# Kernel optimization log

Measured on AMD Instinct MI355X. Metric: run time of the kernel, lower is better.

## Reference

```python
import jax, jax.numpy as jnp
import numpy as np

KH = KW = 3
STRIDE = 1
PAD = 1
DIL = 1


def _conv2d(x, w, b):
    out = jax.lax.conv_general_dilated(
        x, w, (STRIDE, STRIDE), [(PAD, PAD), (PAD, PAD)],
        rhs_dilation=(DIL, DIL), dimension_numbers=('NCHW', 'OIHW', 'NCHW'))
    return out + b[None, :, None, None]


def _bilinear_sample(x, ys, xs):
    # x: [B,C,H,W]; ys, xs: [B,K,Ho,Wo] float sampling coords (zero padding outside)
    B, C, H, W = x.shape
    y0 = jnp.floor(ys)
    x0 = jnp.floor(xs)
    wy1 = ys - y0
    wx1 = xs - x0
    wy0 = 1.0 - wy1
    wx0 = 1.0 - wx1
    x_flat = x.reshape(B, C, H * W)

    def gather(yc, xc):
        valid = (yc >= 0) & (yc <= H - 1) & (xc >= 0) & (xc <= W - 1)
        yi = jnp.clip(yc, 0, H - 1).astype(jnp.int32)
        xi = jnp.clip(xc, 0, W - 1).astype(jnp.int32)
        idx = yi * W + xi  # [B,K,Ho,Wo]
        g = jax.vmap(lambda xb, ib: xb[:, ib.reshape(-1)])(x_flat, idx)
        g = g.reshape(B, C, *idx.shape[1:])  # [B,C,K,Ho,Wo]
        return g * valid[:, None].astype(x.dtype)

    return (gather(y0, x0) * (wy0 * wx0)[:, None]
            + gather(y0, x0 + 1) * (wy0 * wx1)[:, None]
            + gather(y0 + 1, x0) * (wy1 * wx0)[:, None]
            + gather(y0 + 1, x0 + 1) * (wy1 * wx1)[:, None])


def setup_inputs() -> dict:
    key = jax.random.key(0)
    ks = jax.random.split(key, 6)
    B, C, H, W = 8, 256, 64, 64
    Cout = 256
    K = KH * KW
    x = jax.random.normal(ks[0], (B, C, H, W), jnp.float32)
    # small random offset/mask heads (module inits them to zero; random keeps the
    # irregular-gather path exercised with modest, realistic offsets)
    w_offset = jax.random.normal(ks[1], (2 * K, C, KH, KW), jnp.float32) * 0.01
    b_offset = jax.random.normal(ks[2], (2 * K,), jnp.float32) * 0.1
    w_mask = jax.random.normal(ks[3], (K, C, KH, KW), jnp.float32) * 0.01
    b_mask = jnp.zeros((K,), jnp.float32)
    stdv = 1.0 / np.sqrt(C * KH * KW)
    weight = jax.random.uniform(ks[4], (Cout, C, KH, KW), jnp.float32, -stdv, stdv)
    bias = jnp.zeros((Cout,), jnp.float32)
    return {"x": x, "w_offset": w_offset, "b_offset": b_offset,
            "w_mask": w_mask, "b_mask": b_mask, "weight": weight, "bias": bias}


def reference(x, w_offset, b_offset, w_mask, b_mask, weight, bias):
    B, C, H, W = x.shape
    K = KH * KW
    offset = _conv2d(x, w_offset, b_offset)          # [B, 2K, Ho, Wo]
    mask = jax.nn.sigmoid(_conv2d(x, w_mask, b_mask))  # [B, K, Ho, Wo]
    Ho, Wo = offset.shape[2], offset.shape[3]
    off = offset.reshape(B, K, 2, Ho, Wo)
    dy, dx = off[:, :, 0], off[:, :, 1]              # (dy, dx) pairs per kernel tap
    ky = jnp.arange(KH, dtype=x.dtype) * DIL - PAD
    kx = jnp.arange(KW, dtype=x.dtype) * DIL - PAD
    kyf = jnp.repeat(ky, KW)   # [K]
    kxf = jnp.tile(kx, KH)     # [K]
    ys = jnp.arange(Ho, dtype=x.dtype)[None, None, :, None] * STRIDE + kyf[None, :, None, None] + dy
    xs = jnp.arange(Wo, dtype=x.dtype)[None, None, None, :] * STRIDE + kxf[None, :, None, None] + dx
    sampled = _bilinear_sample(x, ys, xs) * mask[:, None]  # [B,C,K,Ho,Wo]
    out = jnp.einsum('bckhw,ock->bohw', sampled, weight.reshape(weight.shape[0], C, K))
    return out + bias[None, :, None, None]
```

## Files before the change

### kernel.cpp

```cpp
#include <hip/hip_runtime.h>
#include <math.h>


typedef __bf16 bf16x8 __attribute__((ext_vector_type(8)));
typedef float  f32x4  __attribute__((ext_vector_type(4)));
typedef float  f32x2  __attribute__((ext_vector_type(2)));
typedef int    i32x4  __attribute__((ext_vector_type(4)));
typedef unsigned short u16x8 __attribute__((ext_vector_type(8)));
typedef unsigned short u16x4 __attribute__((ext_vector_type(4)));

__device__ __forceinline__ unsigned short f2b(float f) {
  return __builtin_bit_cast(unsigned short, (__bf16)f);
}
__device__ __forceinline__ float blo(unsigned u) {
  return __builtin_bit_cast(float, u << 16);
}
__device__ __forceinline__ float bhi(unsigned u) {
  return __builtin_bit_cast(float, u & 0xffff0000u);
}

__global__ __launch_bounds__(256) void transpose_nhwc(const float* __restrict__ x,
                                                      unsigned short* __restrict__ xt) {
  __shared__ float tile[64][65];
  const int bid = blockIdx.x;
  const int b = bid & 7, rem = bid >> 3;
  const int cc = rem & 3, hw0 = (rem >> 2) << 6;
  const int t = threadIdx.x;
  const int a = t & 63, g = t >> 6;
#pragma unroll
  for (int r = 0; r < 16; ++r) {
    int crow = (r << 2) + g;
    tile[crow][a] = x[(((b << 8) + (cc << 6) + crow) << 12) + hw0 + a];
  }
  __syncthreads();
  const int a0 = (t & 15) << 2, gg = t >> 4;
#pragma unroll
  for (int r = 0; r < 4; ++r) {
    int hwr = (r << 4) + gg;
    u16x4 v;
#pragma unroll
    for (int j = 0; j < 4; ++j) v[j] = f2b(tile[a0 + j][hwr]);
    *(u16x4*)&xt[((b << 12) + hw0 + hwr) * 256 + (cc << 6) + a0] = v;
  }
}

__global__ __launch_bounds__(256) void pack_all(const float* __restrict__ w,
                                                const float* __restrict__ wo,
                                                const float* __restrict__ wm,
                                                __bf16* __restrict__ wp,
                                                __bf16* __restrict__ womp) {
  if (blockIdx.x < 2304) {
    int idx = blockIdx.x * 256 + threadIdx.x;
    int o = idx / 2304, rem = idx - o * 2304;
    int c = rem / 9, k = rem - c * 9;
    wp[(((k << 5) + (c >> 3)) * 256 + o) * 8 + (c & 7)] = (__bf16)w[idx];
  } else {
    int idx = (blockIdx.x - 2304) * 256 + threadIdx.x;
    if (idx >= 32 * 256 * 9) return;
    int r = idx / 2304, rem = idx - r * 2304;
    int c = rem / 9, k = rem - c * 9;
    float v = 0.f;
    if (r < 18) v = wo[((r << 8) + c) * 9 + k];
    else if (r < 27) v = wm[(((r - 18) << 8) + c) * 9 + k];
    womp[(((k << 5) + (c >> 3)) * 32 + r) * 8 + (c & 7)] = (__bf16)v;
  }
}

__global__ __launch_bounds__(256) void offset_conv(
    const unsigned short* __restrict__ xt, const __bf16* __restrict__ wp,
    const float* __restrict__ b_off, const float* __restrict__ b_msk,
    float* __restrict__ dyp, float* __restrict__ dxp, float* __restrict__ mkp) {
  const int bi = blockIdx.x & 7, h = blockIdx.x >> 3;
  const int t = threadIdx.x, lane = t & 63, nw = t >> 6;
  const int l16 = lane & 15, lh = lane >> 4;
  __shared__ __align__(16) unsigned short S[2][64 * 64];
  f32x4 acc[2] = {};
  const int sp = t >> 2, sc0 = (t & 3) << 4;
  const int g0 = (t & 3) << 1;
  const int w0 = (sp << 6) + (((g0 ^ (sp & 7)) & 7) << 3);
  const int w1 = (sp << 6) + ((((g0 + 1) ^ (sp & 7)) & 7) << 3);
  const long xb = (long)bi << 20;

  auto LOAD = [&](int it, u16x8* r) {
    const int k = it >> 2, cc = it & 3;
    const int hh = h + k / 3 - 1;
    const int ww = sp + k % 3 - 1;
    const bool valid = (hh >= 0) & (hh < 64) & (ww >= 0) & (ww < 64);
    if (valid) {
      const unsigned short* src = xt + xb + (((hh << 6) + ww) << 8) + (cc << 6) + sc0;
      r[0] = *(const u16x8*)src;
      r[1] = *(const u16x8*)(src + 8);
    } else {
      r[0] = u16x8{}; r[1] = u16x8{};
    }
  };

  auto STEP = [&](int it, const u16x8* r, int buf) {
    unsigned short* Sb = S[buf];
    *(u16x8*)&Sb[w0] = r[0];
    *(u16x8*)&Sb[w1] = r[1];
    __syncthreads();
    const int k = it >> 2, cc = it & 3;
#pragma unroll
    for (int kk = 0; kk < 2; ++kk) {
      const int prow = (nw << 4) + l16;
      const int gi = (kk << 2) | lh;
      bf16x8 bfrag = *(const bf16x8*)&Sb[(prow << 6) + (((gi ^ (prow & 7)) & 7) << 3)];
#pragma unroll
      for (int mf = 0; mf < 2; ++mf) {
        const __bf16* ap = wp + ((((k << 5) + (cc << 3) + (kk << 2) + lh) << 5) + (mf << 4) + l16) * 8;
        bf16x8 af = *(const bf16x8*)ap;
        acc[mf] = __builtin_amdgcn_mfma_f32_16x16x32_bf16(af, bfrag, acc[mf], 0, 0, 0);
      }
    }
  };

  u16x8 rA[2], rB[2];
  LOAD(0, rA);
  for (int it = 0; it < 36; it += 2) {
    LOAD(it + 1, rB);
    STEP(it, rA, 0);
    if (it + 2 < 36) LOAD(it + 2, rA);
    STEP(it + 1, rB, 1);
  }

  const int p = (nw << 4) + l16;
  const int hw = (h << 6) + p;
#pragma unroll
  for (int mf = 0; mf < 2; ++mf) {
#pragma unroll
    for (int r = 0; r < 4; ++r) {
      int row = (mf << 4) + (lh << 2) + r;
      float v = acc[mf][r];
      if (row < 18) {
        v += b_off[row];
        float* dst = (row & 1) ? dxp : dyp;
        dst[(((bi * 9) + (row >> 1)) << 12) + hw] = v;
      } else if (row < 27) {
        int km = row - 18;
        v += b_msk[km];
        mkp[(((bi * 9) + km) << 12) + hw] = 1.f / (1.f + expf(-v));
      }
    }
  }
}

__global__ __launch_bounds__(512, 2) void deform_gemm(
    const unsigned short* __restrict__ xt, const __bf16* __restrict__ wp,
    const float* __restrict__ dyp, const float* __restrict__ dxp,
    const float* __restrict__ mkp, const float* __restrict__ bias,
    float* __restrict__ out) {
  const int bi = blockIdx.x & 7, h = blockIdx.x >> 3;
  const int t = threadIdx.x, lane = t & 63, wv = t >> 6;
  const int l16 = lane & 15, lh = lane >> 4;
  __shared__ __align__(16) unsigned short S[2][64 * 64];
  __shared__ __align__(16) float samp[9][64][8];

  for (int i = t; i < 576; i += 512) {
    int k = i >> 6, p = i & 63;
    int idx = (((bi * 9) + k) << 12) + (h << 6) + p;
    float dy = dyp[idx], dx = dxp[idx], mk = mkp[idx];
    float ys = (float)(h + k / 3 - 1) + dy;
    float xs = (float)(p + k % 3 - 1) + dx;
    float y0f = floorf(ys), x0f = floorf(xs);
    int iy0 = (int)y0f, ix0 = (int)x0f;
    float wy1 = ys - y0f, wx1 = xs - x0f;
    float wy0 = 1.f - wy1, wx0 = 1.f - wx1;
    float w00 = wy0 * wx0 * mk, w01 = wy0 * wx1 * mk;
    float w10 = wy1 * wx0 * mk, w11 = wy1 * wx1 * mk;
    if (iy0 < 0 || iy0 > 63) { w00 = 0.f; w01 = 0.f; }
    if (iy0 < -1 || iy0 > 62) { w10 = 0.f; w11 = 0.f; }
    if (ix0 < 0 || ix0 > 63) { w00 = 0.f; w10 = 0.f; }
    if (ix0 < -1 || ix0 > 62) { w01 = 0.f; w11 = 0.f; }
    const int cy0 = min(max(iy0, 0), 63), cy1 = min(max(iy0 + 1, 0), 63);
    const int cx0 = min(max(ix0, 0), 63), cx1 = min(max(ix0 + 1, 0), 63);
    samp[k][p][0] = w00; samp[k][p][1] = w01;
    samp[k][p][2] = w10; samp[k][p][3] = w11;
    samp[k][p][4] = __builtin_bit_cast(float, (((cy0 << 6) + cx0) << 8));
    samp[k][p][5] = __builtin_bit_cast(float, (((cy0 << 6) + cx1) << 8));
    samp[k][p][6] = __builtin_bit_cast(float, (((cy1 << 6) + cx0) << 8));
    samp[k][p][7] = __builtin_bit_cast(float, (((cy1 << 6) + cx1) << 8));
  }
  __syncthreads();

  f32x4 acc[2][4] = {};
  const int sp = t >> 3;
  const int sc0 = (t & 7) << 3;
  const int wofs = (sp << 6) + ((((t & 7) ^ (sp & 7)) & 7) << 3);
  const unsigned short* xtb = xt + ((long)bi << 20);

  auto GATHER = [&](int it, u16x8* r, f32x4& w4) {
    const int k = it >> 2, cc = it & 3;
    w4 = *(const f32x4*)&samp[k][sp][0];
    i32x4 o4 = __builtin_bit_cast(i32x4, *(const f32x4*)&samp[k][sp][4]);
    const int c0 = (cc << 6) + sc0;
    r[0] = *(const u16x8*)(xtb + o4.x + c0);
    r[1] = *(const u16x8*)(xtb + o4.y + c0);
    r[2] = *(const u16x8*)(xtb + o4.z + c0);
    r[3] = *(const u16x8*)(xtb + o4.w + c0);
  };

  auto STEP = [&](int it, const u16x8* r, const f32x4& w4, int buf) {
    u16x8 sv;
    const unsigned* u0 = (const unsigned*)&r[0];
    const unsigned* u1 = (const unsigned*)&r[1];
    const unsigned* u2 = (const unsigned*)&r[2];
    const unsigned* u3 = (const unsigned*)&r[3];
#pragma unroll
    for (int j = 0; j < 4; ++j) {
      f32x2 a{blo(u0[j]), bhi(u0[j])};
      f32x2 b{blo(u1[j]), bhi(u1[j])};
      f32x2 c{blo(u2[j]), bhi(u2[j])};
      f32x2 d{blo(u3[j]), bhi(u3[j])};
      f32x2 s = a * w4.x;
      s += b * w4.y;
      s += c * w4.z;
      s += d * w4.w;
      sv[2 * j]     = f2b(s.x);
      sv[2 * j + 1] = f2b(s.y);
    }
    *(u16x8*)&S[buf][wofs] = sv;
    __syncthreads();
    const int k = it >> 2, cc = it & 3;
#pragma unroll
    for (int kk = 0; kk < 2; ++kk) {
      bf16x8 bfr[4];
#pragma unroll
      for (int nf = 0; nf < 4; ++nf) {
        const int prow = (nf << 4) + l16;
        const int gi = (kk << 2) | lh;
        bfr[nf] = *(const bf16x8*)&S[buf][(prow << 6) + (((gi ^ (prow & 7)) & 7) << 3)];
      }
#pragma unroll
      for (int mf = 0; mf < 2; ++mf) {
        const int orow = (wv << 5) + (mf << 4) + l16;
        const __bf16* ap = wp + ((((k << 5) + (cc << 3) + (kk << 2) + lh) << 8) + orow) * 8;
        bf16x8 af = *(const bf16x8*)ap;
#pragma unroll
        for (int nf = 0; nf < 4; ++nf)
          acc[mf][nf] = __builtin_amdgcn_mfma_f32_16x16x32_bf16(af, bfr[nf], acc[mf][nf], 0, 0, 0);
      }
    }
  };

  u16x8 rA[4], rB[4];
  f32x4 wA, wB;
  GATHER(0, rA, wA);
  for (int it = 0; it < 36; it += 2) {
    GATHER(it + 1, rB, wB);
    STEP(it, rA, wA, 0);
    if (it + 2 < 36) GATHER(it + 2, rA, wA);
    STEP(it + 1, rB, wB, 1);
  }

#pragma unroll
  for (int mf = 0; mf < 2; ++mf) {
    const int o = (wv << 5) + (mf << 4) + (lh << 2);
    f32x4 bv = *(const f32x4*)(bias + o);
#pragma unroll
    for (int nf = 0; nf < 4; ++nf) {
      const int p = (nf << 4) + l16;
      const int hw = (h << 6) + p;
#pragma unroll
      for (int r = 0; r < 4; ++r)
        out[(((bi << 8) + o + r) << 12) + hw] = acc[mf][nf][r] + bv[r];
    }
  }
}

extern "C" void kernel_launch(void* const* d_in, const int* in_sizes, int n_in,
                              void* d_out, int out_size, void* d_ws, size_t ws_size,
                              hipStream_t stream) {
  (void)in_sizes; (void)n_in; (void)out_size; (void)ws_size;
  const float* x        = (const float*)d_in[0];
  const float* w_offset = (const float*)d_in[1];
  const float* b_offset = (const float*)d_in[2];
  const float* w_mask   = (const float*)d_in[3];
  const float* b_mask   = (const float*)d_in[4];
  const float* weight   = (const float*)d_in[5];
  const float* bias     = (const float*)d_in[6];
  float* out = (float*)d_out;

  char* ws = (char*)d_ws;
  unsigned short* xt = (unsigned short*)(ws);
  __bf16* Wpack  = (__bf16*)(ws + 16777216);
  __bf16* Womp   = (__bf16*)(ws + 17956864);
  float*  dyp    = (float*)(ws + 18104320);
  float*  dxp    = (float*)(ws + 19283968);
  float*  mkp    = (float*)(ws + 20463616);

  transpose_nhwc<<<2048, 256, 0, stream>>>(x, xt);
  pack_all<<<2592, 256, 0, stream>>>(weight, w_offset, w_mask, Wpack, Womp);
  offset_conv<<<512, 256, 0, stream>>>(xt, Womp, b_offset, b_mask, dyp, dxp, mkp);
  deform_gemm<<<512, 512, 0, stream>>>(xt, Wpack, dyp, dxp, mkp, bias, out);
}
```

Before: 103.9 us.

## Fuse offset/mask conv into deformable GEMM kernel and merge prep kernels

Merges the NHWC transpose and weight packing into one prep launch, and moves the offset/mask convolution into the deform GEMM block so offsets and mask stay in shared memory instead of round-tripping through global workspace. This cuts two kernel launches and the global write/read of the dy/dx/mask tensors. In exchange, each 512-thread block now does the small offset conv with 8 waves splitting a 32x64 tile, which adds LDS usage and a serial phase before the gather GEMM.

Result: faster. 92.00 us (-11.4%).

```diff
diff --git a/kernel.cpp b/kernel.cpp
--- a/kernel.cpp
+++ b/kernel.cpp
@@ -19,43 +19,42 @@
   return __builtin_bit_cast(float, u & 0xffff0000u);
 }
 
-__global__ __launch_bounds__(256) void transpose_nhwc(const float* __restrict__ x,
-                                                      unsigned short* __restrict__ xt) {
+__global__ __launch_bounds__(256) void prep(const float* __restrict__ x,
+                                            unsigned short* __restrict__ xt,
+                                            const float* __restrict__ w,
+                                            const float* __restrict__ wo,
+                                            const float* __restrict__ wm,
+                                            __bf16* __restrict__ wp,
+                                            __bf16* __restrict__ womp) {
   __shared__ float tile[64][65];
-  const int bid = blockIdx.x;
-  const int b = bid & 7, rem = bid >> 3;
-  const int cc = rem & 3, hw0 = (rem >> 2) << 6;
   const int t = threadIdx.x;
-  const int a = t & 63, g = t >> 6;
-#pragma unroll
-  for (int r = 0; r < 16; ++r) {
-    int crow = (r << 2) + g;
-    tile[crow][a] = x[(((b << 8) + (cc << 6) + crow) << 12) + hw0 + a];
-  }
-  __syncthreads();
-  const int a0 = (t & 15) << 2, gg = t >> 4;
-#pragma unroll
-  for (int r = 0; r < 4; ++r) {
-    int hwr = (r << 4) + gg;
-    u16x4 v;
-#pragma unroll
-    for (int j = 0; j < 4; ++j) v[j] = f2b(tile[a0 + j][hwr]);
-    *(u16x4*)&xt[((b << 12) + hw0 + hwr) * 256 + (cc << 6) + a0] = v;
-  }
-}
-
-__global__ __launch_bounds__(256) void pack_all(const float* __restrict__ w,
-                                                const float* __restrict__ wo,
-                                                const float* __restrict__ wm,
-                                                __bf16* __restrict__ wp,
-                                                __bf16* __restrict__ womp) {
-  if (blockIdx.x < 2304) {
-    int idx = blockIdx.x * 256 + threadIdx.x;
+  if (blockIdx.x < 2048) {
+    const int bid = blockIdx.x;
+    const int b = bid & 7, rem = bid >> 3;
+    const int cc = rem & 3, hw0 = (rem >> 2) << 6;
+    const int a = t & 63, g = t >> 6;
+#pragma unroll
+    for (int r = 0; r < 16; ++r) {
+      int crow = (r << 2) + g;
+      tile[crow][a] = x[(((b << 8) + (cc << 6) + crow) << 12) + hw0 + a];
+    }
+    __syncthreads();
+    const int a0 = (t & 15) << 2, gg = t >> 4;
+#pragma unroll
+    for (int r = 0; r < 4; ++r) {
+      int hwr = (r << 4) + gg;
+      u16x4 v;
+#pragma unroll
+      for (int j = 0; j < 4; ++j) v[j] = f2b(tile[a0 + j][hwr]);
+      *(u16x4*)&xt[((b << 12) + hw0 + hwr) * 256 + (cc << 6) + a0] = v;
+    }
+  } else if (blockIdx.x < 4352) {
+    int idx = (blockIdx.x - 2048) * 256 + t;
     int o = idx / 2304, rem = idx - o * 2304;
     int c = rem / 9, k = rem - c * 9;
     wp[(((k << 5) + (c >> 3)) * 256 + o) * 8 + (c & 7)] = (__bf16)w[idx];
   } else {
-    int idx = (blockIdx.x - 2304) * 256 + threadIdx.x;
+    int idx = (blockIdx.x - 4352) * 256 + t;
     if (idx >= 32 * 256 * 9) return;
     int r = idx / 2304, rem = idx - r * 2304;
     int c = rem / 9, k = rem - c * 9;
@@ -66,100 +65,80 @@
   }
 }
 
-__global__ __launch_bounds__(256) void offset_conv(
+__global__ __launch_bounds__(512, 2) void deform_fused(
     const unsigned short* __restrict__ xt, const __bf16* __restrict__ wp,
-    const float* __restrict__ b_off, const float* __restrict__ b_msk,
-    float* __restrict__ dyp, float* __restrict__ dxp, float* __restrict__ mkp) {
-  const int bi = blockIdx.x & 7, h = blockIdx.x >> 3;
-  const int t = threadIdx.x, lane = t & 63, nw = t >> 6;
-  const int l16 = lane & 15, lh = lane >> 4;
-  __shared__ __align__(16) unsigned short S[2][64 * 64];
-  f32x4 acc[2] = {};
-  const int sp = t >> 2, sc0 = (t & 3) << 4;
-  const int g0 = (t & 3) << 1;
-  const int w0 = (sp << 6) + (((g0 ^ (sp & 7)) & 7) << 3);
-  const int w1 = (sp << 6) + ((((g0 + 1) ^ (sp & 7)) & 7) << 3);
-  const long xb = (long)bi << 20;
-
-  auto LOAD = [&](int it, u16x8* r) {
-    const int k = it >> 2, cc = it & 3;
-    const int hh = h + k / 3 - 1;
-    const int ww = sp + k % 3 - 1;
-    const bool valid = (hh >= 0) & (hh < 64) & (ww >= 0) & (ww < 64);
-    if (valid) {
-      const unsigned short* src = xt + xb + (((hh << 6) + ww) << 8) + (cc << 6) + sc0;
-      r[0] = *(const u16x8*)src;
-      r[1] = *(const u16x8*)(src + 8);
-    } else {
-      r[0] = u16x8{}; r[1] = u16x8{};
-    }
-  };
-
-  auto STEP = [&](int it, const u16x8* r, int buf) {
-    unsigned short* Sb = S[buf];
-    *(u16x8*)&Sb[w0] = r[0];
-    *(u16x8*)&Sb[w1] = r[1];
-    __syncthreads();
-    const int k = it >> 2, cc = it & 3;
-#pragma unroll
-    for (int kk = 0; kk < 2; ++kk) {
-      const int prow = (nw << 4) + l16;
-      const int gi = (kk << 2) | lh;
-      bf16x8 bfrag = *(const bf16x8*)&Sb[(prow << 6) + (((gi ^ (prow & 7)) & 7) << 3)];
-#pragma unroll
-      for (int mf = 0; mf < 2; ++mf) {
-        const __bf16* ap = wp + ((((k << 5) + (cc << 3) + (kk << 2) + lh) << 5) + (mf << 4) + l16) * 8;
-        bf16x8 af = *(const bf16x8*)ap;
-        acc[mf] = __builtin_amdgcn_mfma_f32_16x16x32_bf16(af, bfrag, acc[mf], 0, 0, 0);
-      }
-    }
-  };
-
-  u16x8 rA[2], rB[2];
-  LOAD(0, rA);
-  for (int it = 0; it < 36; it += 2) {
-    LOAD(it + 1, rB);
-    STEP(it, rA, 0);
-    if (it + 2 < 36) LOAD(it + 2, rA);
-    STEP(it + 1, rB, 1);
-  }
-
-  const int p = (nw << 4) + l16;
-  const int hw = (h << 6) + p;
-#pragma unroll
-  for (int mf = 0; mf < 2; ++mf) {
-#pragma unroll
-    for (int r = 0; r < 4; ++r) {
-      int row = (mf << 4) + (lh << 2) + r;
-      float v = acc[mf][r];
-      if (row < 18) {
-        v += b_off[row];
-        float* dst = (row & 1) ? dxp : dyp;
-        dst[(((bi * 9) + (row >> 1)) << 12) + hw] = v;
-      } else if (row < 27) {
-        int km = row - 18;
-        v += b_msk[km];
-        mkp[(((bi * 9) + km) << 12) + hw] = 1.f / (1.f + expf(-v));
-      }
-    }
-  }
-}
-
-__global__ __launch_bounds__(512, 2) void deform_gemm(
-    const unsigned short* __restrict__ xt, const __bf16* __restrict__ wp,
-    const float* __restrict__ dyp, const float* __restrict__ dxp,
-    const float* __restrict__ mkp, const float* __restrict__ bias,
+    const __bf16* __restrict__ womp, const float* __restrict__ b_off,
+    const float* __restrict__ b_msk, const float* __restrict__ bias,
     float* __restrict__ out) {
   const int bi = blockIdx.x & 7, h = blockIdx.x >> 3;
   const int t = threadIdx.x, lane = t & 63, wv = t >> 6;
   const int l16 = lane & 15, lh = lane >> 4;
   __shared__ __align__(16) unsigned short S[2][64 * 64];
   __shared__ __align__(16) float samp[9][64][8];
+  __shared__ __align__(16) float offm[27][64];
+
+  const int sp = t >> 3;
+  const int sc0 = (t & 7) << 3;
+  const int wofs = (sp << 6) + ((((t & 7) ^ (sp & 7)) & 7) << 3);
+  const unsigned short* xtb = xt + ((long)bi << 20);
+
+  {
+    f32x4 oacc = {};
+    const int mf = wv & 1, nf = wv >> 1;
+
+    auto POLOAD = [&](int it, u16x8* r) {
+      const int k = it >> 2, cc = it & 3;
+      const int hh = h + k / 3 - 1;
+      const int ww = sp + (k % 3) - 1;
+      const bool valid = (hh >= 0) & (hh < 64) & (ww >= 0) & (ww < 64);
+      if (valid)
+        r[0] = *(const u16x8*)(xtb + (((hh << 6) + ww) << 8) + (cc << 6) + sc0);
+      else
+        r[0] = u16x8{};
+    };
+
+    auto POSTEP = [&](int it, const u16x8* r, int buf) {
+      *(u16x8*)&S[buf][wofs] = r[0];
+      __syncthreads();
+      const int k = it >> 2, cc = it & 3;
+#pragma unroll
+      for (int kk = 0; kk < 2; ++kk) {
+        const int prow = (nf << 4) + l16;
+        const int gi = (kk << 2) | lh;
+        bf16x8 bfrag = *(const bf16x8*)&S[buf][(prow << 6) + (((gi ^ (prow & 7)) & 7) << 3)];
+        const __bf16* ap =
+            womp + ((((k << 5) + (cc << 3) + (kk << 2) + lh) << 5) + (mf << 4) + l16) * 8;
+        bf16x8 af = *(const bf16x8*)ap;
+        oacc = __builtin_amdgcn_mfma_f32_16x16x32_bf16(af, bfrag, oacc, 0, 0, 0);
+      }
+    };
+
+    u16x8 pA[1], pB[1];
+    POLOAD(0, pA);
+    for (int it = 0; it < 36; it += 2) {
+      POLOAD(it + 1, pB);
+      POSTEP(it, pA, 0);
+      if (it + 2 < 36) POLOAD(it + 2, pA);
+      POSTEP(it + 1, pB, 1);
+    }
+
+    const int px = (nf << 4) + l16;
+#pragma unroll
+    for (int r = 0; r < 4; ++r) {
+      int row = (mf << 4) + (lh << 2) + r;
+      if (row < 18) {
+        offm[row][px] = oacc[r] + b_off[row];
+      } else if (row < 27) {
+        float v = oacc[r] + b_msk[row - 18];
+        offm[row][px] = 1.f / (1.f + expf(-v));
+      }
+    }
+    __syncthreads();
+  }
 
   for (int i = t; i < 576; i += 512) {
     int k = i >> 6, p = i & 63;
-    int idx = (((bi * 9) + k) << 12) + (h << 6) + p;
-    float dy = dyp[idx], dx = dxp[idx], mk = mkp[idx];
+    float dy = offm[(k << 1)][p], dx = offm[(k << 1) + 1][p], mk = offm[18 + k][p];
     float ys = (float)(h + k / 3 - 1) + dy;
     float xs = (float)(p + k % 3 - 1) + dx;
     float y0f = floorf(ys), x0f = floorf(xs);
@@ -184,10 +163,6 @@
   __syncthreads();
 
   f32x4 acc[2][4] = {};
-  const int sp = t >> 3;
-  const int sc0 = (t & 7) << 3;
-  const int wofs = (sp << 6) + ((((t & 7) ^ (sp & 7)) & 7) << 3);
-  const unsigned short* xtb = xt + ((long)bi << 20);
 
   auto GATHER = [&](int it, u16x8* r, f32x4& w4) {
     const int k = it >> 2, cc = it & 3;
@@ -285,12 +260,7 @@
   unsigned short* xt = (unsigned short*)(ws);
   __bf16* Wpack  = (__bf16*)(ws + 16777216);
   __bf16* Womp   = (__bf16*)(ws + 17956864);
-  float*  dyp    = (float*)(ws + 18104320);
-  float*  dxp    = (float*)(ws + 19283968);
-  float*  mkp    = (float*)(ws + 20463616);
-
-  transpose_nhwc<<<2048, 256, 0, stream>>>(x, xt);
-  pack_all<<<2592, 256, 0, stream>>>(weight, w_offset, w_mask, Wpack, Womp);
-  offset_conv<<<512, 256, 0, stream>>>(xt, Womp, b_offset, b_mask, dyp, dxp, mkp);
-  deform_gemm<<<512, 512, 0, stream>>>(xt, Wpack, dyp, dxp, mkp, bias, out);
-}
+
+  prep<<<4640, 256, 0, stream>>>(x, xt, weight, w_offset, w_mask, Wpack, Womp);
+  deform_fused<<<512, 512, 0, stream>>>(xt, Wpack, Womp, b_offset, b_mask, bias, out);
+}
```
